# Optimization experiments

Hardware: AMD Instinct MI355X
Metric: run time of the kernel (lower is better)

The kernel has to match this reference:

```python
import jax, jax.numpy as jnp
import numpy as np
import itertools, string

# Weight space: 2-layer MLP params, flattened in dict-key order (W1, W2, b1, b2).
SPECS = [(0, 1), (1, 2), (1,), (2,)]
N = 1024            # size of each permutable dim (perm ids 0,1,2)
C_IN, C_OUT = 16, 16
NUM_TERMS = [9, 10, 7, 6]   # equivariant basis terms per output leaf


def _set_partitions(elems):
    if not elems:
        yield []
        return
    first, rest = elems[0], elems[1:]
    for part in _set_partitions(rest):
        for i in range(len(part)):
            yield part[:i] + [part[i] + [first]] + part[i + 1:]
        yield part + [[first]]


def gen_basis(out_spec, in_spec, out_dims, x):
    """All permutation-equivariant basis maps from x (*in_dims, c) to (*out_dims, c).
    Basis elements <-> set partitions of (in,out) axis positions sharing a perm id:
    in-axes in a block are diagonalized; in-only blocks are summed; mixed blocks copy
    the axis to the matching out position; out-only blocks broadcast."""
    pos = ([('in', a, p) for a, p in enumerate(in_spec)]
           + [('out', a, p) for a, p in enumerate(out_spec)])
    by_pid = {}
    for q in pos:
        by_pid.setdefault(q[2], []).append(q)
    parts = [list(_set_partitions(by_pid[p])) for p in sorted(by_pid)]
    terms = []
    for combo in itertools.product(*parts):
        blocks = [b for part in combo for b in part]
        pos2b = {(q[0], q[1]): bi for bi, b in enumerate(blocks) for q in b}
        L = string.ascii_lowercase
        in_sub = ''.join(L[pos2b[('in', a)]] for a in range(len(in_spec)))
        mixed = [bi for bi, b in enumerate(blocks)
                 if any(q[0] == 'in' for q in b) and any(q[0] == 'out' for q in b)]
        out_sub = ''.join(L[bi] for bi in mixed)
        # diagonal over repeated in-axes, sum over in-only blocks; z = channel axis
        t = jnp.einsum(f'{in_sub}z->{out_sub}z', x)
        targets = [min(q[1] for q in blocks[bi] if q[0] == 'out') for bi in mixed]
        t = jnp.transpose(t, list(np.argsort(targets)) + [len(mixed)])
        st = sorted(targets)
        for ax in range(len(out_dims)):
            if ax not in st:
                t = jnp.expand_dims(t, ax)
        t = jnp.broadcast_to(t, tuple(out_dims) + (x.shape[-1],))
        for b in blocks:  # diagonal-embed blocks with >1 out axis (not hit for MLP specs)
            outs = sorted(q[1] for q in b if q[0] == 'out')
            for a1, a2 in zip(outs, outs[1:]):
                n = out_dims[a1]
                sh = [1] * (len(out_dims) + 1)
                sh[a1] = n; sh[a2] = n
                t = t * jnp.eye(n, dtype=x.dtype).reshape(sh)
        terms.append(t)
    return terms


def _forward(flat, thetas, biases):
    outs = []
    for i in range(len(flat)):
        out_dims = flat[i].shape[:-1]
        acc = jnp.zeros(tuple(out_dims) + (C_OUT,), dtype=flat[i].dtype)
        k = 0
        for j in range(len(flat)):
            for term in gen_basis(SPECS[i], SPECS[j], out_dims, flat[j]):
                acc = acc + jnp.einsum('...i,io->...o', term, thetas[i][k])
                k += 1
        outs.append(acc + biases[i])
    return tuple(outs)


def setup_inputs() -> dict:
    key = jax.random.key(0)
    ks = jax.random.split(key, 12)
    inp = {
        'W1': jax.random.normal(ks[0], (N, N, C_IN), jnp.float32),
        'W2': jax.random.normal(ks[1], (N, N, C_IN), jnp.float32),
        'b1': jax.random.normal(ks[2], (N, C_IN), jnp.float32),
        'b2': jax.random.normal(ks[3], (N, C_IN), jnp.float32),
    }
    for i, k in enumerate(NUM_TERMS):
        scale = (1.0 / (C_IN * k)) ** 0.5
        inp[f'theta_{i}'] = scale * jax.random.normal(ks[4 + i], (k, C_IN, C_OUT), jnp.float32)
        inp[f'bias_{i}'] = jnp.zeros((C_OUT,), jnp.float32)
    return inp


def reference(W1, W2, b1, b2, theta_0, theta_1, theta_2, theta_3,
              bias_0, bias_1, bias_2, bias_3):
    return _forward([W1, W2, b1, b2],
                    [theta_0, theta_1, theta_2, theta_3],
                    [bias_0, bias_1, bias_2, bias_3])
```

## Files before the change

kernel.cpp:

```cpp
#include <hip/hip_runtime.h>

#define NDIM 1024
#define CH 16
#define ROW_FLOATS (NDIM * CH)
#define ROW_F4 (ROW_FLOATS / 4)

__global__ __launch_bounds__(256) void k_rowsum(const float* __restrict__ W1,
                                                const float* __restrict__ W2,
                                                float* __restrict__ rowsum) {
    int i = blockIdx.x;
    int z = blockIdx.y;
    const float4* W = (const float4*)((z ? W2 : W1) + (size_t)i * ROW_FLOATS);
    int t = threadIdx.x;
    float4 a = make_float4(0.f, 0.f, 0.f, 0.f);
#pragma unroll 4
    for (int k = 0; k < ROW_F4 / 256; ++k) {
        float4 v = W[t + 256 * k];
        a.x += v.x; a.y += v.y; a.z += v.z; a.w += v.w;
    }
    __shared__ float4 lds[256];
    lds[t] = a;
    __syncthreads();
    if (t < 64) {
        float4 s = lds[t];
#pragma unroll
        for (int o = 1; o < 4; ++o) {
            float4 v = lds[t + 64 * o];
            s.x += v.x; s.y += v.y; s.z += v.z; s.w += v.w;
        }
        lds[t] = s;
    }
    __syncthreads();
    if (t < 4) {
        float4 s = make_float4(0.f, 0.f, 0.f, 0.f);
#pragma unroll
        for (int m = 0; m < 16; ++m) {
            float4 v = lds[t + 4 * m];
            s.x += v.x; s.y += v.y; s.z += v.z; s.w += v.w;
        }
        float* dst = rowsum + ((size_t)z * NDIM + i) * CH + 4 * t;
        dst[0] = s.x; dst[1] = s.y; dst[2] = s.z; dst[3] = s.w;
    }
}

__global__ __launch_bounds__(256) void k_colsum_partial(const float* __restrict__ W1,
                                                        const float* __restrict__ W2,
                                                        float* __restrict__ partial) {
    int t   = threadIdx.x;
    int f4  = t & 31;
    int oct = t >> 5;
    int j0  = blockIdx.x * 8;
    int i0  = blockIdx.y * 512;
    int z   = blockIdx.z;
    const float4* base =
        (const float4*)((z ? W2 : W1) + (size_t)i0 * ROW_FLOATS + (size_t)j0 * CH);
    float4 a = make_float4(0.f, 0.f, 0.f, 0.f);
#pragma unroll 4
    for (int k = 0; k < 64; ++k) {
        int i = 8 * k + oct;
        float4 v = base[(size_t)i * ROW_F4 + f4];
        a.x += v.x; a.y += v.y; a.z += v.z; a.w += v.w;
    }
    __shared__ float4 lds[256];
    lds[t] = a;
    __syncthreads();
    if (t < 32) {
        float4 s = lds[t];
#pragma unroll
        for (int o = 1; o < 8; ++o) {
            float4 v = lds[t + 32 * o];
            s.x += v.x; s.y += v.y; s.z += v.z; s.w += v.w;
        }
        int j  = j0 + (t >> 2);
        int c0 = (t & 3) * 4;
        float* dst = partial + (((size_t)z * 2 + blockIdx.y) * NDIM + j) * CH + c0;
        dst[0] = s.x; dst[1] = s.y; dst[2] = s.z; dst[3] = s.w;
    }
}

__global__ __launch_bounds__(256) void k_sums(const float* __restrict__ rowsum,
                                              const float* __restrict__ b1,
                                              const float* __restrict__ b2,
                                              float* __restrict__ sums) {
    int tgt = blockIdx.x;
    const float* src = (tgt == 0) ? rowsum
                     : (tgt == 1) ? rowsum + 16384
                     : (tgt == 2) ? b1 : b2;
    int t = threadIdx.x;
    const float4* s4 = (const float4*)src;
    float4 a = make_float4(0.f, 0.f, 0.f, 0.f);
#pragma unroll
    for (int k = 0; k < 16; ++k) {
        float4 v = s4[t + 256 * k];
        a.x += v.x; a.y += v.y; a.z += v.z; a.w += v.w;
    }
    __shared__ float4 lds[256];
    lds[t] = a;
    __syncthreads();
    if (t < 64) {
        float4 s = lds[t];
#pragma unroll
        for (int o = 1; o < 4; ++o) {
            float4 v = lds[t + 64 * o];
            s.x += v.x; s.y += v.y; s.z += v.z; s.w += v.w;
        }
        lds[t] = s;
    }
    __syncthreads();
    if (t < 4) {
        float4 s = make_float4(0.f, 0.f, 0.f, 0.f);
#pragma unroll
        for (int m = 0; m < 16; ++m) {
            float4 v = lds[t + 4 * m];
            s.x += v.x; s.y += v.y; s.z += v.z; s.w += v.w;
        }
        float* dst = sums + tgt * 16 + 4 * t;
        dst[0] = s.x; dst[1] = s.y; dst[2] = s.z; dst[3] = s.w;
    }
}

__global__ __launch_bounds__(256) void k_smalls(const float* __restrict__ rowsum,
                                                const float* __restrict__ partial,
                                                const float* __restrict__ sums,
                                                const float* __restrict__ b1,
                                                const float* __restrict__ b2,
                                                const float* __restrict__ th0,
                                                const float* __restrict__ th1,
                                                const float* __restrict__ th2,
                                                const float* __restrict__ th3,
                                                const float* __restrict__ bias0,
                                                const float* __restrict__ bias1,
                                                const float* __restrict__ bias2,
                                                const float* __restrict__ bias3,
                                                float* __restrict__ R0, float* __restrict__ C0,
                                                float* __restrict__ R1, float* __restrict__ C1,
                                                float* __restrict__ out2, float* __restrict__ out3) {
    int gt = blockIdx.x * 256 + threadIdx.x;
    int i = gt >> 4, o = gt & 15;
    const float* rs1 = rowsum + i * 16;
    const float* rs2 = rowsum + 16384 + i * 16;
    const float* b1i = b1 + i * 16;
    const float* b2i = b2 + i * 16;
    float cs1[16], cs2[16];
#pragma unroll
    for (int c = 0; c < 16; ++c) {
        cs1[c] = partial[i * 16 + c]         + partial[16384 + i * 16 + c];
        cs2[c] = partial[32768 + i * 16 + c] + partial[49152 + i * 16 + c];
    }
    float r0 = 0.f, c0a = 0.f, r1 = 0.f, c1a = 0.f, o2 = 0.f, o3 = 0.f;
    float k0 = 0.f, k1 = 0.f, k2 = 0.f, k3 = 0.f;
#pragma unroll
    for (int c = 0; c < 16; ++c) {
        float sW1 = sums[c], sW2 = sums[16 + c], sb1 = sums[32 + c], sb2 = sums[48 + c];
        r0  += rs1[c] * th0[(1 * 16 + c) * 16 + o];
        c0a += cs1[c] * th0[(2 * 16 + c) * 16 + o]
             + rs2[c] * th0[(4 * 16 + c) * 16 + o]
             + b1i[c] * th0[(6 * 16 + c) * 16 + o];
        k0  += sW1 * th0[(3 * 16 + c) * 16 + o] + sW2 * th0[(5 * 16 + c) * 16 + o]
             + sb1 * th0[(7 * 16 + c) * 16 + o] + sb2 * th0[(8 * 16 + c) * 16 + o];
        r1  += cs1[c] * th1[(0 * 16 + c) * 16 + o]
             + rs2[c] * th1[(3 * 16 + c) * 16 + o]
             + b1i[c] * th1[(6 * 16 + c) * 16 + o];
        c1a += cs2[c] * th1[(4 * 16 + c) * 16 + o]
             + b2i[c] * th1[(8 * 16 + c) * 16 + o];
        k1  += sW1 * th1[(1 * 16 + c) * 16 + o] + sW2 * th1[(5 * 16 + c) * 16 + o]
             + sb1 * th1[(7 * 16 + c) * 16 + o] + sb2 * th1[(9 * 16 + c) * 16 + o];
        o2  += cs1[c] * th2[(0 * 16 + c) * 16 + o]
             + rs2[c] * th2[(2 * 16 + c) * 16 + o]
             + b1i[c] * th2[(4 * 16 + c) * 16 + o];
        k2  += sW1 * th2[(1 * 16 + c) * 16 + o] + sW2 * th2[(3 * 16 + c) * 16 + o]
             + sb1 * th2[(5 * 16 + c) * 16 + o] + sb2 * th2[(6 * 16 + c) * 16 + o];
        o3  += cs2[c] * th3[(1 * 16 + c) * 16 + o]
             + b2i[c] * th3[(4 * 16 + c) * 16 + o];
        k3  += sW1 * th3[(0 * 16 + c) * 16 + o] + sW2 * th3[(2 * 16 + c) * 16 + o]
             + sb1 * th3[(3 * 16 + c) * 16 + o] + sb2 * th3[(5 * 16 + c) * 16 + o];
    }
    R0[gt]   = r0;
    C0[gt]   = c0a + k0 + bias0[o];
    R1[gt]   = r1;
    C1[gt]   = c1a + k1 + bias1[o];
    out2[gt] = o2 + k2 + bias2[o];
    out3[gt] = o3 + k3 + bias3[o];
}

__global__ __launch_bounds__(256) void k_main(const float* __restrict__ W1,
                                              const float* __restrict__ W2,
                                              const float* __restrict__ R0,
                                              const float* __restrict__ C0,
                                              const float* __restrict__ R1,
                                              const float* __restrict__ C1,
                                              const float* __restrict__ th0,
                                              const float* __restrict__ th1,
                                              float* __restrict__ out0,
                                              float* __restrict__ out1) {
    int z = blockIdx.z;
    const float* W  = z ? W2 : W1;
    const float* R  = z ? R1 : R0;
    const float* Cc = z ? C1 : C0;
    const float* TH = z ? th1 : th0;
    float* out      = z ? out1 : out0;

    int t = threadIdx.x;
    int i = blockIdx.y;
    int j = blockIdx.x * 256 + t;

    __shared__ float th[256];
    __shared__ float r[16];
    th[t] = TH[t];
    if (t < 16) r[t] = R[i * 16 + t];
    __syncthreads();

    size_t base = ((size_t)i * NDIM + j) * CH;
    const float4* xp = (const float4*)(W + base);
    float4 x0 = xp[0], x1 = xp[1], x2 = xp[2], x3 = xp[3];
    float x[16] = {x0.x, x0.y, x0.z, x0.w, x1.x, x1.y, x1.z, x1.w,
                   x2.x, x2.y, x2.z, x2.w, x3.x, x3.y, x3.z, x3.w};

    const float4* cj = (const float4*)(Cc + j * 16);
    float4 c0 = cj[0], c1 = cj[1], c2 = cj[2], c3 = cj[3];
    float acc[16] = {c0.x, c0.y, c0.z, c0.w, c1.x, c1.y, c1.z, c1.w,
                     c2.x, c2.y, c2.z, c2.w, c3.x, c3.y, c3.z, c3.w};
#pragma unroll
    for (int o = 0; o < 16; ++o) acc[o] += r[o];
#pragma unroll
    for (int c = 0; c < 16; ++c) {
        float xv = x[c];
#pragma unroll
        for (int o = 0; o < 16; ++o) acc[o] += xv * th[c * 16 + o];
    }
    float4* op = (float4*)(out + base);
    op[0] = make_float4(acc[0],  acc[1],  acc[2],  acc[3]);
    op[1] = make_float4(acc[4],  acc[5],  acc[6],  acc[7]);
    op[2] = make_float4(acc[8],  acc[9],  acc[10], acc[11]);
    op[3] = make_float4(acc[12], acc[13], acc[14], acc[15]);
}

extern "C" void kernel_launch(void* const* d_in, const int* in_sizes, int n_in,
                              void* d_out, int out_size, void* d_ws, size_t ws_size,
                              hipStream_t stream) {
    const float* W1    = (const float*)d_in[0];
    const float* W2    = (const float*)d_in[1];
    const float* b1    = (const float*)d_in[2];
    const float* b2    = (const float*)d_in[3];
    const float* th0   = (const float*)d_in[4];
    const float* bias0 = (const float*)d_in[5];
    const float* th1   = (const float*)d_in[6];
    const float* bias1 = (const float*)d_in[7];
    const float* th2   = (const float*)d_in[8];
    const float* bias2 = (const float*)d_in[9];
    const float* th3   = (const float*)d_in[10];
    const float* bias3 = (const float*)d_in[11];

    float* out  = (float*)d_out;
    float* out0 = out;
    float* out1 = out + (size_t)NDIM * NDIM * CH;
    float* out2 = out1 + (size_t)NDIM * NDIM * CH;
    float* out3 = out2 + (size_t)NDIM * CH;

    float* ws      = (float*)d_ws;
    float* rowsum  = ws;
    float* partial = ws + 32768;
    float* sums    = ws + 98304;
    float* R0      = ws + 98368;
    float* C0      = R0 + 16384;
    float* R1      = C0 + 16384;
    float* C1      = R1 + 16384;

    k_rowsum<<<dim3(NDIM, 2), dim3(256), 0, stream>>>(W1, W2, rowsum);
    k_colsum_partial<<<dim3(128, 2, 2), dim3(256), 0, stream>>>(W1, W2, partial);
    k_sums<<<dim3(4), dim3(256), 0, stream>>>(rowsum, b1, b2, sums);
    k_smalls<<<dim3(64), dim3(256), 0, stream>>>(rowsum, partial, sums, b1, b2,
                                                 th0, th1, th2, th3,
                                                 bias0, bias1, bias2, bias3,
                                                 R0, C0, R1, C1, out2, out3);
    k_main<<<dim3(4, NDIM, 2), dim3(256), 0, stream>>>(W1, W2, R0, C0, R1, C1,
                                                       th0 ,
                                                       th1 + 2 * 256 ,
                                                       out0, out1);
}
```

Before: 106.5 us.

## Fuse row and column sum reductions into a single pass over W

Adds a tiled kernel that reads each 64x64 tile of W1/W2 once. It accumulates column partials in registers and row partials through wave shuffles plus LDS, then a small finalize kernel combines the 16 partials per output. This replaces the separate rowsum and colsum kernels, which each streamed the full weight tensors, and is meant to cut one full read of W. It needs a larger workspace and falls back to the old path when the workspace is too small; the extra partial buffers and shuffles add some overhead.

```diff
diff --git a/kernel.cpp b/kernel.cpp
--- a/kernel.cpp
+++ b/kernel.cpp
@@ -4,6 +4,75 @@
 #define CH 16
 #define ROW_FLOATS (NDIM * CH)
 #define ROW_F4 (ROW_FLOATS / 4)
+
+__device__ inline float4 f4add(float4 a, float4 b) {
+    return make_float4(a.x + b.x, a.y + b.y, a.z + b.z, a.w + b.w);
+}
+__device__ inline float4 f4shfl_xor(float4 v, int m) {
+    return make_float4(__shfl_xor(v.x, m), __shfl_xor(v.y, m),
+                       __shfl_xor(v.z, m), __shfl_xor(v.w, m));
+}
+
+__global__ __launch_bounds__(256) void k_fused(const float* __restrict__ W1,
+                                               const float* __restrict__ W2,
+                                               float* __restrict__ rowpart,
+                                               float* __restrict__ colpart) {
+    int t  = threadIdx.x;
+    int bj = blockIdx.x, bi = blockIdx.y, z = blockIdx.z;
+    int j0 = bj * 64, i0 = bi * 64;
+    const float4* base = (const float4*)(z ? W2 : W1)
+                       + (size_t)i0 * ROW_F4 + j0 * 4 + t;
+    __shared__ float rowacc[4][64][16];
+    int w = t >> 6, lane = t & 63;
+    float4 colacc = make_float4(0.f, 0.f, 0.f, 0.f);
+#pragma unroll 4
+    for (int k = 0; k < 64; ++k) {
+        float4 v = base[(size_t)k * ROW_F4];
+        colacc = f4add(colacc, v);
+        float4 vr = v;
+        vr = f4add(vr, f4shfl_xor(vr, 4));
+        vr = f4add(vr, f4shfl_xor(vr, 8));
+        vr = f4add(vr, f4shfl_xor(vr, 16));
+        vr = f4add(vr, f4shfl_xor(vr, 32));
+        if (lane < 4) {
+            rowacc[w][k][lane * 4 + 0] = vr.x;
+            rowacc[w][k][lane * 4 + 1] = vr.y;
+            rowacc[w][k][lane * 4 + 2] = vr.z;
+            rowacc[w][k][lane * 4 + 3] = vr.w;
+        }
+    }
+    int jl = t >> 2, cq = t & 3;
+    {
+        size_t coff = (((size_t)z * 16 + bi) * NDIM + (j0 + jl)) * CH + cq * 4;
+        *(float4*)(colpart + coff) = colacc;
+    }
+    __syncthreads();
+    {
+        int r = t >> 2;
+        const float4* ra = (const float4*)&rowacc[0][0][0];
+        float4 s = f4add(f4add(ra[(0 * 64 + r) * 4 + cq], ra[(1 * 64 + r) * 4 + cq]),
+                         f4add(ra[(2 * 64 + r) * 4 + cq], ra[(3 * 64 + r) * 4 + cq]));
+        size_t roff = (((size_t)z * 16 + bj) * NDIM + (i0 + r)) * CH + cq * 4;
+        *(float4*)(rowpart + roff) = s;
+    }
+}
+
+__global__ __launch_bounds__(256) void k_finalize(const float* __restrict__ rowpart,
+                                                  const float* __restrict__ colpart,
+                                                  float* __restrict__ rowsumF,
+                                                  float* __restrict__ colsumF) {
+    int gt  = blockIdx.x * 256 + threadIdx.x;
+    int sel = gt >> 15;
+    int rem = gt & 32767;
+    const float* src = sel ? colpart : rowpart;
+    float* dst       = sel ? colsumF : rowsumF;
+    int z = rem >> 14, idx = rem & 16383;
+    const float* p = src + (size_t)z * 16 * 16384 + idx;
+    float s = 0.f;
+#pragma unroll
+    for (int ch = 0; ch < 16; ++ch) s += p[ch * 16384];
+    dst[rem] = s;
+}
 
 __global__ __launch_bounds__(256) void k_rowsum(const float* __restrict__ W1,
                                                 const float* __restrict__ W2,
@@ -16,7 +85,7 @@
 #pragma unroll 4
     for (int k = 0; k < ROW_F4 / 256; ++k) {
         float4 v = W[t + 256 * k];
-        a.x += v.x; a.y += v.y; a.z += v.z; a.w += v.w;
+        a = f4add(a, v);
     }
     __shared__ float4 lds[256];
     lds[t] = a;
@@ -24,20 +93,14 @@
     if (t < 64) {
         float4 s = lds[t];
 #pragma unroll
-        for (int o = 1; o < 4; ++o) {
-            float4 v = lds[t + 64 * o];
-            s.x += v.x; s.y += v.y; s.z += v.z; s.w += v.w;
-        }
+        for (int o = 1; o < 4; ++o) s = f4add(s, lds[t + 64 * o]);
         lds[t] = s;
     }
     __syncthreads();
     if (t < 4) {
         float4 s = make_float4(0.f, 0.f, 0.f, 0.f);
 #pragma unroll
-        for (int m = 0; m < 16; ++m) {
-            float4 v = lds[t + 4 * m];
-            s.x += v.x; s.y += v.y; s.z += v.z; s.w += v.w;
-        }
+        for (int m = 0; m < 16; ++m) s = f4add(s, lds[t + 4 * m]);
         float* dst = rowsum + ((size_t)z * NDIM + i) * CH + 4 * t;
         dst[0] = s.x; dst[1] = s.y; dst[2] = s.z; dst[3] = s.w;
     }
@@ -58,8 +121,7 @@
 #pragma unroll 4
     for (int k = 0; k < 64; ++k) {
         int i = 8 * k + oct;
-        float4 v = base[(size_t)i * ROW_F4 + f4];
-        a.x += v.x; a.y += v.y; a.z += v.z; a.w += v.w;
+        a = f4add(a, base[(size_t)i * ROW_F4 + f4]);
     }
     __shared__ float4 lds[256];
     lds[t] = a;
@@ -67,10 +129,7 @@
     if (t < 32) {
         float4 s = lds[t];
 #pragma unroll
-        for (int o = 1; o < 8; ++o) {
-            float4 v = lds[t + 32 * o];
-            s.x += v.x; s.y += v.y; s.z += v.z; s.w += v.w;
-        }
+        for (int o = 1; o < 8; ++o) s = f4add(s, lds[t + 32 * o]);
         int j  = j0 + (t >> 2);
         int c0 = (t & 3) * 4;
         float* dst = partial + (((size_t)z * 2 + blockIdx.y) * NDIM + j) * CH + c0;
@@ -90,63 +149,50 @@
     const float4* s4 = (const float4*)src;
     float4 a = make_float4(0.f, 0.f, 0.f, 0.f);
 #pragma unroll
-    for (int k = 0; k < 16; ++k) {
-        float4 v = s4[t + 256 * k];
-        a.x += v.x; a.y += v.y; a.z += v.z; a.w += v.w;
-    }
+    for (int k = 0; k < 16; ++k) a = f4add(a, s4[t + 256 * k]);
     __shared__ float4 lds[256];
     lds[t] = a;
     __syncthreads();
     if (t < 64) {
         float4 s = lds[t];
 #pragma unroll
-        for (int o = 1; o < 4; ++o) {
-            float4 v = lds[t + 64 * o];
-            s.x += v.x; s.y += v.y; s.z += v.z; s.w += v.w;
-        }
+        for (int o = 1; o < 4; ++o) s = f4add(s, lds[t + 64 * o]);
         lds[t] = s;
     }
     __syncthreads();
     if (t < 4) {
         float4 s = make_float4(0.f, 0.f, 0.f, 0.f);
 #pragma unroll
-        for (int m = 0; m < 16; ++m) {
-            float4 v = lds[t + 4 * m];
-            s.x += v.x; s.y += v.y; s.z += v.z; s.w += v.w;
-        }
+        for (int m = 0; m < 16; ++m) s = f4add(s, lds[t + 4 * m]);
         float* dst = sums + tgt * 16 + 4 * t;
         dst[0] = s.x; dst[1] = s.y; dst[2] = s.z; dst[3] = s.w;
     }
 }
 
-__global__ __launch_bounds__(256) void k_smalls(const float* __restrict__ rowsum,
-                                                const float* __restrict__ partial,
-                                                const float* __restrict__ sums,
-                                                const float* __restrict__ b1,
-                                                const float* __restrict__ b2,
-                                                const float* __restrict__ th0,
-                                                const float* __restrict__ th1,
-                                                const float* __restrict__ th2,
-                                                const float* __restrict__ th3,
-                                                const float* __restrict__ bias0,
-                                                const float* __restrict__ bias1,
-                                                const float* __restrict__ bias2,
-                                                const float* __restrict__ bias3,
-                                                float* __restrict__ R0, float* __restrict__ C0,
-                                                float* __restrict__ R1, float* __restrict__ C1,
-                                                float* __restrict__ out2, float* __restrict__ out3) {
+__global__ __launch_bounds__(256) void k_smalls2(const float* __restrict__ rowsum,
+                                                 const float* __restrict__ colsum,
+                                                 const float* __restrict__ sums,
+                                                 const float* __restrict__ b1,
+                                                 const float* __restrict__ b2,
+                                                 const float* __restrict__ th0,
+                                                 const float* __restrict__ th1,
+                                                 const float* __restrict__ th2,
+                                                 const float* __restrict__ th3,
+                                                 const float* __restrict__ bias0,
+                                                 const float* __restrict__ bias1,
+                                                 const float* __restrict__ bias2,
+                                                 const float* __restrict__ bias3,
+                                                 float* __restrict__ R0, float* __restrict__ C0,
+                                                 float* __restrict__ R1, float* __restrict__ C1,
+                                                 float* __restrict__ out2, float* __restrict__ out3) {
     int gt = blockIdx.x * 256 + threadIdx.x;
     int i = gt >> 4, o = gt & 15;
     const float* rs1 = rowsum + i * 16;
     const float* rs2 = rowsum + 16384 + i * 16;
+    const float* cs1 = colsum + i * 16;
+    const float* cs2 = colsum + 16384 + i * 16;
     const float* b1i = b1 + i * 16;
     const float* b2i = b2 + i * 16;
-    float cs1[16], cs2[16];
-#pragma unroll
-    for (int c = 0; c < 16; ++c) {
-        cs1[c] = partial[i * 16 + c]         + partial[16384 + i * 16 + c];
-        cs2[c] = partial[32768 + i * 16 + c] + partial[49152 + i * 16 + c];
-    }
     float r0 = 0.f, c0a = 0.f, r1 = 0.f, c1a = 0.f, o2 = 0.f, o3 = 0.f;
     float k0 = 0.f, k1 = 0.f, k2 = 0.f, k3 = 0.f;
 #pragma unroll
@@ -183,6 +229,70 @@
     out3[gt] = o3 + k3 + bias3[o];
 }
 
+__global__ __launch_bounds__(256) void k_smalls(const float* __restrict__ rowsum,
+                                                const float* __restrict__ partial,
+                                                const float* __restrict__ sums,
+                                                const float* __restrict__ b1,
+                                                const float* __restrict__ b2,
+                                                const float* __restrict__ th0,
+                                                const float* __restrict__ th1,
+                                                const float* __restrict__ th2,
+                                                const float* __restrict__ th3,
+                                                const float* __restrict__ bias0,
+                                                const float* __restrict__ bias1,
+                                                const float* __restrict__ bias2,
+                                                const float* __restrict__ bias3,
+                                                float* __restrict__ R0, float* __restrict__ C0,
+                                                float* __restrict__ R1, float* __restrict__ C1,
+                                                float* __restrict__ out2, float* __restrict__ out3) {
+    int gt = blockIdx.x * 256 + threadIdx.x;
+    int i = gt >> 4, o = gt & 15;
+    const float* rs1 = rowsum + i * 16;
+    const float* rs2 = rowsum + 16384 + i * 16;
+    const float* b1i = b1 + i * 16;
+    const float* b2i = b2 + i * 16;
+    float cs1[16], cs2[16];
+#pragma unroll
+    for (int c = 0; c < 16; ++c) {
+        cs1[c] = partial[i * 16 + c]         + partial[16384 + i * 16 + c];
+        cs2[c] = partial[32768 + i * 16 + c] + partial[49152 + i * 16 + c];
+    }
+    float r0 = 0.f, c0a = 0.f, r1 = 0.f, c1a = 0.f, o2 = 0.f, o3 = 0.f;
+    float k0 = 0.f, k1 = 0.f, k2 = 0.f, k3 = 0.f;
+#pragma unroll
+    for (int c = 0; c < 16; ++c) {
+        float sW1 = sums[c], sW2 = sums[16 + c], sb1 = sums[32 + c], sb2 = sums[48 + c];
+        r0  += rs1[c] * th0[(1 * 16 + c) * 16 + o];
+        c0a += cs1[c] * th0[(2 * 16 + c) * 16 + o]
+             + rs2[c] * th0[(4 * 16 + c) * 16 + o]
+             + b1i[c] * th0[(6 * 16 + c) * 16 + o];
+        k0  += sW1 * th0[(3 * 16 + c) * 16 + o] + sW2 * th0[(5 * 16 + c) * 16 + o]
+             + sb1 * th0[(7 * 16 + c) * 16 + o] + sb2 * th0[(8 * 16 + c) * 16 + o];
+        r1  += cs1[c] * th1[(0 * 16 + c) * 16 + o]
+             + rs2[c] * th1[(3 * 16 + c) * 16 + o]
+             + b1i[c] * th1[(6 * 16 + c) * 16 + o];
+        c1a += cs2[c] * th1[(4 * 16 + c) * 16 + o]
+             + b2i[c] * th1[(8 * 16 + c) * 16 + o];
+        k1  += sW1 * th1[(1 * 16 + c) * 16 + o] + sW2 * th1[(5 * 16 + c) * 16 + o]
+             + sb1 * th1[(7 * 16 + c) * 16 + o] + sb2 * th1[(9 * 16 + c) * 16 + o];
+        o2  += cs1[c] * th2[(0 * 16 + c) * 16 + o]
+             + rs2[c] * th2[(2 * 16 + c) * 16 + o]
+             + b1i[c] * th2[(4 * 16 + c) * 16 + o];
+        k2  += sW1 * th2[(1 * 16 + c) * 16 + o] + sW2 * th2[(3 * 16 + c) * 16 + o]
+             + sb1 * th2[(5 * 16 + c) * 16 + o] + sb2 * th2[(6 * 16 + c) * 16 + o];
+        o3  += cs2[c] * th3[(1 * 16 + c) * 16 + o]
+             + b2i[c] * th3[(4 * 16 + c) * 16 + o];
+        k3  += sW1 * th3[(0 * 16 + c) * 16 + o] + sW2 * th3[(2 * 16 + c) * 16 + o]
+             + sb1 * th3[(3 * 16 + c) * 16 + o] + sb2 * th3[(5 * 16 + c) * 16 + o];
+    }
+    R0[gt]   = r0;
+    C0[gt]   = c0a + k0 + bias0[o];
+    R1[gt]   = r1;
+    C1[gt]   = c1a + k1 + bias1[o];
+    out2[gt] = o2 + k2 + bias2[o];
+    out3[gt] = o3 + k3 + bias3[o];
+}
+
 __global__ __launch_bounds__(256) void k_main(const float* __restrict__ W1,
                                               const float* __restrict__ W2,
                                               const float* __restrict__ R0,
@@ -257,24 +367,49 @@
     float* out2 = out1 + (size_t)NDIM * NDIM * CH;
     float* out3 = out2 + (size_t)NDIM * CH;
 
-    float* ws      = (float*)d_ws;
-    float* rowsum  = ws;
-    float* partial = ws + 32768;
-    float* sums    = ws + 98304;
-    float* R0      = ws + 98368;
-    float* C0      = R0 + 16384;
-    float* R1      = C0 + 16384;
-    float* C1      = R1 + 16384;
-
-    k_rowsum<<<dim3(NDIM, 2), dim3(256), 0, stream>>>(W1, W2, rowsum);
-    k_colsum_partial<<<dim3(128, 2, 2), dim3(256), 0, stream>>>(W1, W2, partial);
-    k_sums<<<dim3(4), dim3(256), 0, stream>>>(rowsum, b1, b2, sums);
-    k_smalls<<<dim3(64), dim3(256), 0, stream>>>(rowsum, partial, sums, b1, b2,
-                                                 th0, th1, th2, th3,
-                                                 bias0, bias1, bias2, bias3,
-                                                 R0, C0, R1, C1, out2, out3);
-    k_main<<<dim3(4, NDIM, 2), dim3(256), 0, stream>>>(W1, W2, R0, C0, R1, C1,
-                                                       th0 ,
-                                                       th1 + 2 * 256 ,
-                                                       out0, out1);
-}
+    float* ws = (float*)d_ws;
+
+    const size_t FUSED_NEED = (size_t)1179712 * 4;
+
+    if (ws_size >= FUSED_NEED) {
+        float* rowpart = ws;
+        float* colpart = ws + 524288;
+        float* rowsumF = ws + 1048576;
+        float* colsumF = ws + 1081344;
+        float* sums    = ws + 1114112;
+        float* R0      = ws + 1114176;
+        float* C0      = R0 + 16384;
+        float* R1      = C0 + 16384;
+        float* C1      = R1 + 16384;
+
+        k_fused<<<dim3(16, 16, 2), dim3(256), 0, stream>>>(W1, W2, rowpart, colpart);
+        k_finalize<<<dim3(256), dim3(256), 0, stream>>>(rowpart, colpart, rowsumF, colsumF);
+        k_sums<<<dim3(4), dim3(256), 0, stream>>>(rowsumF, b1, b2, sums);
+        k_smalls2<<<dim3(64), dim3(256), 0, stream>>>(rowsumF, colsumF, sums, b1, b2,
+                                                      th0, th1, th2, th3,
+                                                      bias0, bias1, bias2, bias3,
+                                                      R0, C0, R1, C1, out2, out3);
+        k_main<<<dim3(4, NDIM, 2), dim3(256), 0, stream>>>(W1, W2, R0, C0, R1, C1,
+                                                           th0, th1 + 2 * 256,
+                                                           out0, out1);
+    } else {
+        float* rowsum  = ws;
+        float* partial = ws + 32768;
+        float* sums    = ws + 98304;
+        float* R0      = ws + 98368;
+        float* C0      = R0 + 16384;
+        float* R1      = C0 + 16384;
+        float* C1      = R1 + 16384;
+
+        k_rowsum<<<dim3(NDIM, 2), dim3(256), 0, stream>>>(W1, W2, rowsum);
+        k_colsum_partial<<<dim3(128, 2, 2), dim3(256), 0, stream>>>(W1, W2, partial);
+        k_sums<<<dim3(4), dim3(256), 0, stream>>>(rowsum, b1, b2, sums);
+        k_smalls<<<dim3(64), dim3(256), 0, stream>>>(rowsum, partial, sums, b1, b2,
+                                                     th0, th1, th2, th3,
+                                                     bias0, bias1, bias2, bias3,
+                                                     R0, C0, R1, C1, out2, out3);
+        k_main<<<dim3(4, NDIM, 2), dim3(256), 0, stream>>>(W1, W2, R0, C0, R1, C1,
+                                                           th0, th1 + 2 * 256,
+                                                           out0, out1);
+    }
+}
```

Measured after the change: 107.0 us. About the same (+0.5%).

## Fuse row and column sums into one tiled pass over W1/W2

Applied to the files above, without the earlier changes.

Replaces the separate row-sum and column-sum kernels, which each read all of W1 and W2, with one kernel over 64x64 tiles. That kernel accumulates column partials in registers and row partials through wave shuffles plus LDS, so the big weight tensors are read once instead of twice. A small finalize kernel then reduces the 16 per-tile partials. The partials are staged in the output buffer before k_main overwrites it, which adds one kernel launch and some extra traffic.

```diff
diff --git a/kernel.cpp b/kernel.cpp
--- a/kernel.cpp
+++ b/kernel.cpp
@@ -5,77 +5,73 @@
 #define ROW_FLOATS (NDIM * CH)
 #define ROW_F4 (ROW_FLOATS / 4)
 
-__global__ __launch_bounds__(256) void k_rowsum(const float* __restrict__ W1,
-                                                const float* __restrict__ W2,
-                                                float* __restrict__ rowsum) {
-    int i = blockIdx.x;
-    int z = blockIdx.y;
-    const float4* W = (const float4*)((z ? W2 : W1) + (size_t)i * ROW_FLOATS);
-    int t = threadIdx.x;
-    float4 a = make_float4(0.f, 0.f, 0.f, 0.f);
-#pragma unroll 4
-    for (int k = 0; k < ROW_F4 / 256; ++k) {
-        float4 v = W[t + 256 * k];
-        a.x += v.x; a.y += v.y; a.z += v.z; a.w += v.w;
-    }
-    __shared__ float4 lds[256];
-    lds[t] = a;
-    __syncthreads();
-    if (t < 64) {
-        float4 s = lds[t];
-#pragma unroll
-        for (int o = 1; o < 4; ++o) {
-            float4 v = lds[t + 64 * o];
-            s.x += v.x; s.y += v.y; s.z += v.z; s.w += v.w;
-        }
-        lds[t] = s;
-    }
-    __syncthreads();
-    if (t < 4) {
-        float4 s = make_float4(0.f, 0.f, 0.f, 0.f);
-#pragma unroll
-        for (int m = 0; m < 16; ++m) {
-            float4 v = lds[t + 4 * m];
-            s.x += v.x; s.y += v.y; s.z += v.z; s.w += v.w;
-        }
-        float* dst = rowsum + ((size_t)z * NDIM + i) * CH + 4 * t;
-        dst[0] = s.x; dst[1] = s.y; dst[2] = s.z; dst[3] = s.w;
-    }
-}
-
-__global__ __launch_bounds__(256) void k_colsum_partial(const float* __restrict__ W1,
-                                                        const float* __restrict__ W2,
-                                                        float* __restrict__ partial) {
-    int t   = threadIdx.x;
-    int f4  = t & 31;
-    int oct = t >> 5;
-    int j0  = blockIdx.x * 8;
-    int i0  = blockIdx.y * 512;
-    int z   = blockIdx.z;
-    const float4* base =
-        (const float4*)((z ? W2 : W1) + (size_t)i0 * ROW_FLOATS + (size_t)j0 * CH);
-    float4 a = make_float4(0.f, 0.f, 0.f, 0.f);
+__device__ inline float4 f4add(float4 a, float4 b) {
+    return make_float4(a.x + b.x, a.y + b.y, a.z + b.z, a.w + b.w);
+}
+__device__ inline float4 f4shfl_xor(float4 v, int m) {
+    return make_float4(__shfl_xor(v.x, m), __shfl_xor(v.y, m),
+                       __shfl_xor(v.z, m), __shfl_xor(v.w, m));
+}
+
+__global__ __launch_bounds__(256) void k_fused(const float* __restrict__ W1,
+                                               const float* __restrict__ W2,
+                                               float* __restrict__ rowpart,
+                                               float* __restrict__ colpart) {
+    int t  = threadIdx.x;
+    int bj = blockIdx.x, bi = blockIdx.y, z = blockIdx.z;
+    int j0 = bj * 64, i0 = bi * 64;
+    const float4* base = (const float4*)(z ? W2 : W1)
+                       + (size_t)i0 * ROW_F4 + j0 * 4 + t;
+    __shared__ float rowacc[4][64][16];
+    int w = t >> 6, lane = t & 63;
+    float4 colacc = make_float4(0.f, 0.f, 0.f, 0.f);
 #pragma unroll 4
     for (int k = 0; k < 64; ++k) {
-        int i = 8 * k + oct;
-        float4 v = base[(size_t)i * ROW_F4 + f4];
-        a.x += v.x; a.y += v.y; a.z += v.z; a.w += v.w;
-    }
-    __shared__ float4 lds[256];
-    lds[t] = a;
-    __syncthreads();
-    if (t < 32) {
-        float4 s = lds[t];
-#pragma unroll
-        for (int o = 1; o < 8; ++o) {
-            float4 v = lds[t + 32 * o];
-            s.x += v.x; s.y += v.y; s.z += v.z; s.w += v.w;
+        float4 v = base[(size_t)k * ROW_F4];
+        colacc = f4add(colacc, v);
+        float4 vr = v;
+        vr = f4add(vr, f4shfl_xor(vr, 4));
+        vr = f4add(vr, f4shfl_xor(vr, 8));
+        vr = f4add(vr, f4shfl_xor(vr, 16));
+        vr = f4add(vr, f4shfl_xor(vr, 32));
+        if (lane < 4) {
+            rowacc[w][k][lane * 4 + 0] = vr.x;
+            rowacc[w][k][lane * 4 + 1] = vr.y;
+            rowacc[w][k][lane * 4 + 2] = vr.z;
+            rowacc[w][k][lane * 4 + 3] = vr.w;
         }
-        int j  = j0 + (t >> 2);
-        int c0 = (t & 3) * 4;
-        float* dst = partial + (((size_t)z * 2 + blockIdx.y) * NDIM + j) * CH + c0;
-        dst[0] = s.x; dst[1] = s.y; dst[2] = s.z; dst[3] = s.w;
-    }
+    }
+    int jl = t >> 2, cq = t & 3;
+    {
+        size_t coff = (((size_t)z * 16 + bi) * NDIM + (j0 + jl)) * CH + cq * 4;
+        *(float4*)(colpart + coff) = colacc;
+    }
+    __syncthreads();
+    {
+        int r = t >> 2;
+        const float4* ra = (const float4*)&rowacc[0][0][0];
+        float4 s = f4add(f4add(ra[(0 * 64 + r) * 4 + cq], ra[(1 * 64 + r) * 4 + cq]),
+                         f4add(ra[(2 * 64 + r) * 4 + cq], ra[(3 * 64 + r) * 4 + cq]));
+        size_t roff = (((size_t)z * 16 + bj) * NDIM + (i0 + r)) * CH + cq * 4;
+        *(float4*)(rowpart + roff) = s;
+    }
+}
+
+__global__ __launch_bounds__(256) void k_finalize(const float* __restrict__ rowpart,
+                                                  const float* __restrict__ colpart,
+                                                  float* __restrict__ rowsumF,
+                                                  float* __restrict__ colsumF) {
+    int gt  = blockIdx.x * 256 + threadIdx.x;
+    int sel = gt >> 15;
+    int rem = gt & 32767;
+    const float* src = sel ? colpart : rowpart;
+    float* dst       = sel ? colsumF : rowsumF;
+    int z = rem >> 14, idx = rem & 16383;
+    const float* p = src + (size_t)z * 16 * 16384 + idx;
+    float s = 0.f;
+#pragma unroll
+    for (int ch = 0; ch < 16; ++ch) s += p[ch * 16384];
+    dst[rem] = s;
 }
 
 __global__ __launch_bounds__(256) void k_sums(const float* __restrict__ rowsum,
@@ -90,37 +86,28 @@
     const float4* s4 = (const float4*)src;
     float4 a = make_float4(0.f, 0.f, 0.f, 0.f);
 #pragma unroll
-    for (int k = 0; k < 16; ++k) {
-        float4 v = s4[t + 256 * k];
-        a.x += v.x; a.y += v.y; a.z += v.z; a.w += v.w;
-    }
+    for (int k = 0; k < 16; ++k) a = f4add(a, s4[t + 256 * k]);
     __shared__ float4 lds[256];
     lds[t] = a;
     __syncthreads();
     if (t < 64) {
         float4 s = lds[t];
 #pragma unroll
-        for (int o = 1; o < 4; ++o) {
-            float4 v = lds[t + 64 * o];
-            s.x += v.x; s.y += v.y; s.z += v.z; s.w += v.w;
-        }
+        for (int o = 1; o < 4; ++o) s = f4add(s, lds[t + 64 * o]);
         lds[t] = s;
     }
     __syncthreads();
     if (t < 4) {
         float4 s = make_float4(0.f, 0.f, 0.f, 0.f);
 #pragma unroll
-        for (int m = 0; m < 16; ++m) {
-            float4 v = lds[t + 4 * m];
-            s.x += v.x; s.y += v.y; s.z += v.z; s.w += v.w;
-        }
+        for (int m = 0; m < 16; ++m) s = f4add(s, lds[t + 4 * m]);
         float* dst = sums + tgt * 16 + 4 * t;
         dst[0] = s.x; dst[1] = s.y; dst[2] = s.z; dst[3] = s.w;
     }
 }
 
 __global__ __launch_bounds__(256) void k_smalls(const float* __restrict__ rowsum,
-                                                const float* __restrict__ partial,
+                                                const float* __restrict__ colsum,
                                                 const float* __restrict__ sums,
                                                 const float* __restrict__ b1,
                                                 const float* __restrict__ b2,
@@ -139,14 +126,10 @@
     int i = gt >> 4, o = gt & 15;
     const float* rs1 = rowsum + i * 16;
     const float* rs2 = rowsum + 16384 + i * 16;
+    const float* cs1 = colsum + i * 16;
+    const float* cs2 = colsum + 16384 + i * 16;
     const float* b1i = b1 + i * 16;
     const float* b2i = b2 + i * 16;
-    float cs1[16], cs2[16];
-#pragma unroll
-    for (int c = 0; c < 16; ++c) {
-        cs1[c] = partial[i * 16 + c]         + partial[16384 + i * 16 + c];
-        cs2[c] = partial[32768 + i * 16 + c] + partial[49152 + i * 16 + c];
-    }
     float r0 = 0.f, c0a = 0.f, r1 = 0.f, c1a = 0.f, o2 = 0.f, o3 = 0.f;
     float k0 = 0.f, k1 = 0.f, k2 = 0.f, k3 = 0.f;
 #pragma unroll
@@ -257,24 +240,26 @@
     float* out2 = out1 + (size_t)NDIM * NDIM * CH;
     float* out3 = out2 + (size_t)NDIM * CH;
 
+    float* rowpart = out0;
+    float* colpart = out0 + 524288;
+
     float* ws      = (float*)d_ws;
-    float* rowsum  = ws;
-    float* partial = ws + 32768;
-    float* sums    = ws + 98304;
-    float* R0      = ws + 98368;
+    float* rowsumF = ws;
+    float* colsumF = ws + 32768;
+    float* sums    = ws + 65536;
+    float* R0      = ws + 65600;
     float* C0      = R0 + 16384;
     float* R1      = C0 + 16384;
     float* C1      = R1 + 16384;
 
-    k_rowsum<<<dim3(NDIM, 2), dim3(256), 0, stream>>>(W1, W2, rowsum);
-    k_colsum_partial<<<dim3(128, 2, 2), dim3(256), 0, stream>>>(W1, W2, partial);
-    k_sums<<<dim3(4), dim3(256), 0, stream>>>(rowsum, b1, b2, sums);
-    k_smalls<<<dim3(64), dim3(256), 0, stream>>>(rowsum, partial, sums, b1, b2,
+    k_fused<<<dim3(16, 16, 2), dim3(256), 0, stream>>>(W1, W2, rowpart, colpart);
+    k_finalize<<<dim3(256), dim3(256), 0, stream>>>(rowpart, colpart, rowsumF, colsumF);
+    k_sums<<<dim3(4), dim3(256), 0, stream>>>(rowsumF, b1, b2, sums);
+    k_smalls<<<dim3(64), dim3(256), 0, stream>>>(rowsumF, colsumF, sums, b1, b2,
                                                  th0, th1, th2, th3,
                                                  bias0, bias1, bias2, bias3,
                                                  R0, C0, R1, C1, out2, out3);
     k_main<<<dim3(4, NDIM, 2), dim3(256), 0, stream>>>(W1, W2, R0, C0, R1, C1,
-                                                       th0 ,
-                                                       th1 + 2 * 256 ,
+                                                       th0, th1 + 2 * 256,
                                                        out0, out1);
 }
```

After: 104.1 us. -2.2%, faster.
